# Optimization experiments

Measured on AMD Instinct MI355X. Metric: run time of the kernel, lower is better.

Reference implementation:

```python
import jax, jax.numpy as jnp
import numpy as np

HEADS = 4
DIM_HEAD = 32
DIM = 128
HIDDEN = HEADS * DIM_HEAD  # 128
SCALE = 10
EPS = 1e-12  # matches F.normalize default eps


def l2_norm(t):
    # normalize along last axis (heads axis after the port's reshape)
    n = jnp.sqrt(jnp.sum(t * t, axis=-1, keepdims=True))
    return t / jnp.maximum(n, EPS)


def setup_inputs() -> dict:
    key = jax.random.key(0)
    k1, k2, k3 = jax.random.split(key, 3)
    b, h, w = 4, 16, 256
    x = jax.random.normal(k1, (b, h, w, DIM), dtype=jnp.float32)
    # 1x1 conv kernels collapse to dense matrices on the channel axis
    w_qkv = jax.random.normal(k2, (DIM, 3 * HIDDEN), dtype=jnp.float32) / np.sqrt(DIM).astype(np.float32)
    w_out = jax.random.normal(k3, (HIDDEN, DIM), dtype=jnp.float32) / np.sqrt(HIDDEN).astype(np.float32)
    b_out = jnp.zeros((DIM,), dtype=jnp.float32)
    return {"x": x, "w_qkv": w_qkv, "w_out": w_out, "b_out": b_out}


def reference(x, w_qkv, w_out, b_out):
    b, h, w, c = x.shape
    n = h * w
    # 1x1 conv (no bias) -> qkv, split on channel axis
    qkv = jnp.einsum('bhwc,cf->bhwf', x, w_qkv)
    q, k, v = jnp.split(qkv, 3, axis=-1)
    # faithful port reshape: (b, h, w, hidden) -> (b, dim_head, n, heads)
    q = q.reshape(b, -1, n, HEADS)
    k = k.reshape(b, -1, n, HEADS)
    v = v.reshape(b, -1, n, HEADS)
    q = l2_norm(q)  # computed but unused downstream, as in the source
    k = l2_norm(k)
    # sim: contract over dim_head axis -> (b, n, n, heads)
    sim = jnp.einsum('bhdn,bhen->bden', k, v) * SCALE
    attn = jax.nn.softmax(sim, axis=-2)
    # out: contract attn with v over spatial axis -> (b, n, dim_head, heads)
    out = jnp.einsum('bedh,bndh->benh', attn, v)
    out = out.reshape(b, h, w, HIDDEN)
    # final 1x1 conv with bias
    return jnp.einsum('bhwf,fo->bhwo', out, w_out) + b_out
```

## Files before the change

kernel.cpp:

```cpp
#include <hip/hip_runtime.h>
#include <math.h>


#define SEQ 4096
#define PAIR_ELEMS (SEQ * 32)

typedef __attribute__((ext_vector_type(8))) short bf16x8;
typedef __attribute__((ext_vector_type(4))) float f32x4;

static __device__ __forceinline__ unsigned short f2bf(float x) {
    unsigned u = __float_as_uint(x);
    u += 0x7fffu + ((u >> 16) & 1u);
    return (unsigned short)(u >> 16);
}
static __device__ __forceinline__ float bf2f(unsigned short h) {
    return __uint_as_float(((unsigned)h) << 16);
}

__global__ __launch_bounds__(256) void kv_kernel(const float* __restrict__ x,
                                                 const float* __restrict__ wqkv,
                                                 unsigned short* __restrict__ Qhi,
                                                 unsigned short* __restrict__ Qlo,
                                                 unsigned short* __restrict__ Mhi,
                                                 unsigned short* __restrict__ Mlo,
                                                 unsigned short* __restrict__ Mpv) {
    __shared__ __align__(16) float xs[32][128];
    __shared__ __align__(8) unsigned short vstage[32][128];

    const int b    = blockIdx.x >> 7;
    const int p7   = blockIdx.x & 127;
    const int t    = threadIdx.x;
    const int half = t >> 7;
    const int u    = t & 127;
    const int q    = u & 31;
    const int rg   = u >> 5;
    const int woff = 128 + (half << 7) + (q << 2);

    {
        const float* xb = x + ((size_t)(b * SEQ + p7)) * 128;
#pragma unroll
        for (int uu = 0; uu < 4; ++uu) {
            int idx = t + (uu << 8);
            int j   = idx >> 5;
            int c4  = idx & 31;
            *(float4*)&xs[j][c4 * 4] =
                *(const float4*)(xb + (size_t)j * (128 * 128) + c4 * 4);
        }
    }
    __syncthreads();

    float acc[8][4];
#pragma unroll
    for (int jr = 0; jr < 8; ++jr)
#pragma unroll
        for (int a = 0; a < 4; ++a) acc[jr][a] = 0.f;

    float4 wA[4], wB[4];
#pragma unroll
    for (int i = 0; i < 4; ++i)
        wA[i] = *(const float4*)(wqkv + (size_t)i * 384 + woff);

    auto gstep = [&](float4 (&wcur)[4], float4 (&wnxt)[4], int i4) {
        const int i4n = (i4 + 4) & 127;
#pragma unroll
        for (int i = 0; i < 4; ++i)
            wnxt[i] = *(const float4*)(wqkv + (size_t)(i4n + i) * 384 + woff);
#pragma unroll
        for (int jr = 0; jr < 8; ++jr) {
            float4 xv = *(const float4*)&xs[8 * rg + jr][i4];
            acc[jr][0] = fmaf(xv.x, wcur[0].x, acc[jr][0]);
            acc[jr][1] = fmaf(xv.x, wcur[0].y, acc[jr][1]);
            acc[jr][2] = fmaf(xv.x, wcur[0].z, acc[jr][2]);
            acc[jr][3] = fmaf(xv.x, wcur[0].w, acc[jr][3]);
            acc[jr][0] = fmaf(xv.y, wcur[1].x, acc[jr][0]);
            acc[jr][1] = fmaf(xv.y, wcur[1].y, acc[jr][1]);
            acc[jr][2] = fmaf(xv.y, wcur[1].z, acc[jr][2]);
            acc[jr][3] = fmaf(xv.y, wcur[1].w, acc[jr][3]);
            acc[jr][0] = fmaf(xv.z, wcur[2].x, acc[jr][0]);
            acc[jr][1] = fmaf(xv.z, wcur[2].y, acc[jr][1]);
            acc[jr][2] = fmaf(xv.z, wcur[2].z, acc[jr][2]);
            acc[jr][3] = fmaf(xv.z, wcur[2].w, acc[jr][3]);
            acc[jr][0] = fmaf(xv.w, wcur[3].x, acc[jr][0]);
            acc[jr][1] = fmaf(xv.w, wcur[3].y, acc[jr][1]);
            acc[jr][2] = fmaf(xv.w, wcur[3].z, acc[jr][2]);
            acc[jr][3] = fmaf(xv.w, wcur[3].w, acc[jr][3]);
        }
    };
    for (int i4 = 0; i4 < 128; i4 += 8) {
        gstep(wA, wB, i4);
        gstep(wB, wA, i4 + 4);
    }

    const int pairbase = b << 2;
    const int de = (p7 << 5) + q;

    if (half == 0) {
        float qn[8][4];
#pragma unroll
        for (int jr = 0; jr < 8; ++jr) {
            float s = acc[jr][0] * acc[jr][0] + acc[jr][1] * acc[jr][1]
                    + acc[jr][2] * acc[jr][2] + acc[jr][3] * acc[jr][3];
            float inv = 14.426950408889634f / fmaxf(sqrtf(s), 1e-12f);
#pragma unroll
            for (int a = 0; a < 4; ++a) qn[jr][a] = acc[jr][a] * inv;
        }
#pragma unroll
        for (int a = 0; a < 4; ++a) {
            unsigned hi[4], lo[4];
#pragma unroll
            for (int j2 = 0; j2 < 4; ++j2) {
                float v0 = qn[2 * j2][a], v1 = qn[2 * j2 + 1][a];
                unsigned short h0 = f2bf(v0), h1 = f2bf(v1);
                hi[j2] = (unsigned)h0 | ((unsigned)h1 << 16);
                lo[j2] = (unsigned)f2bf(v0 - bf2f(h0))
                       | ((unsigned)f2bf(v1 - bf2f(h1)) << 16);
            }
            size_t off = (size_t)(pairbase + a) * PAIR_ELEMS + (size_t)de * 32 + 8 * rg;
            *(uint4*)(Qhi + off) = make_uint4(hi[0], hi[1], hi[2], hi[3]);
            *(uint4*)(Qlo + off) = make_uint4(lo[0], lo[1], lo[2], lo[3]);
        }
    } else {
#pragma unroll
        for (int a = 0; a < 4; ++a) {
            unsigned hi[4], lo[4];
#pragma unroll
            for (int j2 = 0; j2 < 4; ++j2) {
                float v0 = acc[2 * j2][a], v1 = acc[2 * j2 + 1][a];
                unsigned short h0 = f2bf(v0), h1 = f2bf(v1);
                hi[j2] = (unsigned)h0 | ((unsigned)h1 << 16);
                lo[j2] = (unsigned)f2bf(v0 - bf2f(h0))
                       | ((unsigned)f2bf(v1 - bf2f(h1)) << 16);
            }
            size_t off = (size_t)(pairbase + a) * PAIR_ELEMS + (size_t)de * 32 + 8 * rg;
            *(uint4*)(Mhi + off) = make_uint4(hi[0], hi[1], hi[2], hi[3]);
            *(uint4*)(Mlo + off) = make_uint4(lo[0], lo[1], lo[2], lo[3]);
        }
#pragma unroll
        for (int jr = 0; jr < 8; ++jr) {
            unsigned short h0 = f2bf(acc[jr][0]);
            unsigned short h1 = f2bf(acc[jr][1]);
            unsigned short h2 = f2bf(acc[jr][2]);
            unsigned short h3 = f2bf(acc[jr][3]);
            *(uint2*)&vstage[8 * rg + jr][4 * q] =
                make_uint2((unsigned)h0 | ((unsigned)h1 << 16),
                           (unsigned)h2 | ((unsigned)h3 << 16));
        }
    }
    __syncthreads();

    unsigned* mpv32 = (unsigned*)Mpv;
#pragma unroll
    for (int uu = 0; uu < 8; ++uu) {
        int task = t + (uu << 8);
        int r  = task & 15;
        int jj = (task >> 4) & 31;
        int aa = task >> 9;
        unsigned lo = vstage[jj][(r << 2) + aa];
        unsigned hi = vstage[jj][(r << 2) + aa + 64];
        int pr = (b << 2) + aa;
        size_t dst = (size_t)pr * (PAIR_ELEMS / 2) + (size_t)jj * (SEQ / 2)
                   + ((size_t)(p7 >> 1) << 5) + (r << 1) + (p7 & 1);
        mpv32[dst] = lo | (hi << 16);
    }
}

__global__ __launch_bounds__(256, 2) void attn_kernel(const unsigned short* __restrict__ Qhi,
                                                      const unsigned short* __restrict__ Qlo,
                                                      const unsigned short* __restrict__ Mhi,
                                                      const unsigned short* __restrict__ Mlo,
                                                      const unsigned short* __restrict__ Mpv,
                                                      unsigned short* __restrict__ outb) {
    __shared__ __align__(16) unsigned short Plds[4][32][72];

    const int bid  = blockIdx.x;
    const int pair = ((bid & 7) << 1) + (bid >> 8);
    const int dblk = (bid & 255) >> 3;
    const int t    = threadIdx.x;
    const int wid  = t >> 6;
    const int lane = t & 63;
    const int col  = lane & 15;
    const int g    = lane >> 4;
    const int d0   = dblk * 128 + wid * 32;

    const size_t pb = (size_t)pair * PAIR_ELEMS;

    bf16x8 ah[2], al[2];
#pragma unroll
    for (int s = 0; s < 2; ++s) {
        size_t o = pb + (size_t)(d0 + 16 * s + col) * 32 + g * 8;
        ah[s] = *(const bf16x8*)(Qhi + o);
        al[s] = *(const bf16x8*)(Qlo + o);
    }

    const unsigned short* mh = Mhi + pb;
    const unsigned short* ml = Mlo + pb;
    const unsigned short* mp = Mpv + pb;
    const f32x4 z = {0.f, 0.f, 0.f, 0.f};

    float rmax[2][4];
#pragma unroll
    for (int s = 0; s < 2; ++s)
#pragma unroll
        for (int r = 0; r < 4; ++r) rmax[s][r] = -3e38f;

    {
        bf16x8 pA[4], pB[4];
#pragma unroll
        for (int cc = 0; cc < 4; ++cc)
            pA[cc] = *(const bf16x8*)(mh + (size_t)(16 * cc + col) * 32 + g * 8);

        auto sweep = [&](bf16x8 (&cur)[4], bf16x8 (&nxt)[4], int e0) {
            const int en = (e0 + 64) & (SEQ - 1);
#pragma unroll
            for (int cc = 0; cc < 4; ++cc)
                nxt[cc] = *(const bf16x8*)(mh + (size_t)(en + 16 * cc + col) * 32 + g * 8);
#pragma unroll
            for (int cc = 0; cc < 4; ++cc) {
#pragma unroll
                for (int s = 0; s < 2; ++s) {
                    f32x4 sv = __builtin_amdgcn_mfma_f32_16x16x32_bf16(ah[s], cur[cc], z, 0, 0, 0);
#pragma unroll
                    for (int r = 0; r < 4; ++r) rmax[s][r] = fmaxf(rmax[s][r], sv[r]);
                }
            }
        };
        for (int e0 = 0; e0 < SEQ; e0 += 128) {
            sweep(pA, pB, e0);
            sweep(pB, pA, e0 + 64);
        }
    }
#pragma unroll
    for (int s = 0; s < 2; ++s)
#pragma unroll
        for (int r = 0; r < 4; ++r) {
            float m = rmax[s][r];
            m = fmaxf(m, __shfl_xor(m, 1));
            m = fmaxf(m, __shfl_xor(m, 2));
            m = fmaxf(m, __shfl_xor(m, 4));
            m = fmaxf(m, __shfl_xor(m, 8));
            rmax[s][r] = m;
        }
    f32x4 minit[2];
#pragma unroll
    for (int s = 0; s < 2; ++s)
        minit[s] = (f32x4){-rmax[s][0], -rmax[s][1], -rmax[s][2], -rmax[s][3]};

    f32x4 O[2][2];
    float lsum[2][4];
#pragma unroll
    for (int s = 0; s < 2; ++s) {
#pragma unroll
        for (int r = 0; r < 4; ++r) lsum[s][r] = 0.f;
#pragma unroll
        for (int nh = 0; nh < 2; ++nh) O[s][nh] = (f32x4){0.f, 0.f, 0.f, 0.f};
    }

    {
        bf16x8 tA[12], tB[12];
#pragma unroll
        for (int cc = 0; cc < 4; ++cc) {
            size_t ro = (size_t)(16 * cc + col) * 32 + g * 8;
            tA[cc]     = *(const bf16x8*)(mh + ro);
            tA[4 + cc] = *(const bf16x8*)(ml + ro);
        }
#pragma unroll
        for (int h = 0; h < 2; ++h)
#pragma unroll
            for (int nh = 0; nh < 2; ++nh)
                tA[8 + 2 * h + nh] =
                    *(const bf16x8*)(mp + (size_t)(16 * nh + col) * SEQ + 32 * h + g * 8);

        auto flash = [&](bf16x8 (&cur)[12], bf16x8 (&nxt)[12], int e0) {
            const int en = (e0 + 64) & (SEQ - 1);
#pragma unroll
            for (int cc = 0; cc < 4; ++cc) {
                size_t ro = (size_t)(en + 16 * cc + col) * 32 + g * 8;
                nxt[cc]     = *(const bf16x8*)(mh + ro);
                nxt[4 + cc] = *(const bf16x8*)(ml + ro);
            }
#pragma unroll
            for (int h = 0; h < 2; ++h)
#pragma unroll
                for (int nh = 0; nh < 2; ++nh)
                    nxt[8 + 2 * h + nh] =
                        *(const bf16x8*)(mp + (size_t)(16 * nh + col) * SEQ
                                         + en + 32 * h + g * 8);

            f32x4 S[2][4];
#pragma unroll
            for (int cc = 0; cc < 4; ++cc) {
#pragma unroll
                for (int s = 0; s < 2; ++s) {
                    f32x4 tac = __builtin_amdgcn_mfma_f32_16x16x32_bf16(ah[s], cur[4 + cc], minit[s], 0, 0, 0);
                    tac = __builtin_amdgcn_mfma_f32_16x16x32_bf16(al[s], cur[cc], tac, 0, 0, 0);
                    S[s][cc] = __builtin_amdgcn_mfma_f32_16x16x32_bf16(ah[s], cur[cc], tac, 0, 0, 0);
                }
            }
#pragma unroll
            for (int s = 0; s < 2; ++s) {
#pragma unroll
                for (int r = 0; r < 4; ++r) {
                    float p0 = __builtin_amdgcn_exp2f(S[s][0][r]);
                    float p1 = __builtin_amdgcn_exp2f(S[s][1][r]);
                    float p2 = __builtin_amdgcn_exp2f(S[s][2][r]);
                    float p3 = __builtin_amdgcn_exp2f(S[s][3][r]);
                    lsum[s][r] += (p0 + p1) + (p2 + p3);
                    unsigned w0 = (unsigned)f2bf(p0) | ((unsigned)f2bf(p1) << 16);
                    unsigned w1 = (unsigned)f2bf(p2) | ((unsigned)f2bf(p3) << 16);
                    unsigned* dst = (unsigned*)&Plds[wid][16 * s + 4 * g + r][col * 4];
                    dst[0] = w0;
                    dst[1] = w1;
                }
            }
            asm volatile("s_waitcnt lgkmcnt(0)" ::: "memory");
            __builtin_amdgcn_sched_barrier(0);
#pragma unroll
            for (int h = 0; h < 2; ++h) {
                bf16x8 pa[2];
#pragma unroll
                for (int s = 0; s < 2; ++s)
                    pa[s] = *(const bf16x8*)&Plds[wid][16 * s + col][32 * h + g * 8];
                O[0][0] = __builtin_amdgcn_mfma_f32_16x16x32_bf16(pa[0], cur[8 + 2 * h + 0], O[0][0], 0, 0, 0);
                O[0][1] = __builtin_amdgcn_mfma_f32_16x16x32_bf16(pa[0], cur[8 + 2 * h + 1], O[0][1], 0, 0, 0);
                O[1][0] = __builtin_amdgcn_mfma_f32_16x16x32_bf16(pa[1], cur[8 + 2 * h + 0], O[1][0], 0, 0, 0);
                O[1][1] = __builtin_amdgcn_mfma_f32_16x16x32_bf16(pa[1], cur[8 + 2 * h + 1], O[1][1], 0, 0, 0);
            }
            asm volatile("" ::: "memory");
        };
        for (int e0 = 0; e0 < SEQ; e0 += 128) {
            flash(tA, tB, e0);
            flash(tB, tA, e0 + 64);
        }
    }

#pragma unroll
    for (int s = 0; s < 2; ++s)
#pragma unroll
        for (int r = 0; r < 4; ++r) {
            float l = lsum[s][r];
            l += __shfl_xor(l, 1);
            l += __shfl_xor(l, 2);
            l += __shfl_xor(l, 4);
            l += __shfl_xor(l, 8);
            lsum[s][r] = l;
        }

    const int bb = pair >> 2;
    const int aa = pair & 3;
#pragma unroll
    for (int s = 0; s < 2; ++s) {
#pragma unroll
        for (int r = 0; r < 4; ++r) {
            int d = d0 + 16 * s + 4 * g + r;
            float inv = 1.0f / lsum[s][r];
#pragma unroll
            for (int nh = 0; nh < 2; ++nh) {
                int n2 = 16 * nh + col;
                outb[((size_t)(bb * SEQ + d)) * 128 + n2 * 4 + aa] =
                    f2bf(O[s][nh][r] * inv);
            }
        }
    }
}

__global__ __launch_bounds__(256) void out_kernel(const unsigned short* __restrict__ opre,
                                                  const float* __restrict__ wout,
                                                  const float* __restrict__ bout,
                                                  float* __restrict__ y) {
    __shared__ __align__(16) float xs[8][128];
    const int r0 = blockIdx.x * 8;
    const int t  = threadIdx.x;
    {
        const unsigned* src = (const unsigned*)(opre + (size_t)r0 * 128);
        unsigned v0 = src[t * 2], v1 = src[t * 2 + 1];
        float* dst = &xs[0][0] + t * 4;
        dst[0] = bf2f((unsigned short)(v0 & 0xffff));
        dst[1] = bf2f((unsigned short)(v0 >> 16));
        dst[2] = bf2f((unsigned short)(v1 & 0xffff));
        dst[3] = bf2f((unsigned short)(v1 >> 16));
    }
    __syncthreads();

    const int c  = t & 127;
    const int rh = (t >> 7) * 4;
    float acc[4] = {0.f, 0.f, 0.f, 0.f};

    for (int i = 0; i < 128; i += 4) {
        float w0 = wout[(i + 0) * 128 + c];
        float w1 = wout[(i + 1) * 128 + c];
        float w2 = wout[(i + 2) * 128 + c];
        float w3 = wout[(i + 3) * 128 + c];
#pragma unroll
        for (int p = 0; p < 4; ++p) {
            float4 xp = *(const float4*)&xs[rh + p][i];
            acc[p] = fmaf(xp.x, w0, acc[p]);
            acc[p] = fmaf(xp.y, w1, acc[p]);
            acc[p] = fmaf(xp.z, w2, acc[p]);
            acc[p] = fmaf(xp.w, w3, acc[p]);
        }
    }
    float bb = bout[c];
#pragma unroll
    for (int p = 0; p < 4; ++p) {
        y[((size_t)(r0 + rh + p)) * 128 + c] = acc[p] + bb;
    }
}

extern "C" void kernel_launch(void* const* d_in, const int* in_sizes, int n_in,
                              void* d_out, int out_size, void* d_ws, size_t ws_size,
                              hipStream_t stream) {
    const float* x    = (const float*)d_in[0];
    const float* wqkv = (const float*)d_in[1];
    const float* wout = (const float*)d_in[2];
    const float* bout = (const float*)d_in[3];
    float* y = (float*)d_out;

    unsigned short* Qhi = (unsigned short*)d_ws;
    unsigned short* Qlo = Qhi + (size_t)16 * PAIR_ELEMS;
    unsigned short* Mhi = Qlo + (size_t)16 * PAIR_ELEMS;
    unsigned short* Mlo = Mhi + (size_t)16 * PAIR_ELEMS;
    unsigned short* Mpv = Mlo + (size_t)16 * PAIR_ELEMS;
    unsigned short* outb = Mpv + (size_t)16 * PAIR_ELEMS;

    kv_kernel<<<512, 256, 0, stream>>>(x, wqkv, Qhi, Qlo, Mhi, Mlo, Mpv);
    attn_kernel<<<512, 256, 0, stream>>>(Qhi, Qlo, Mhi, Mlo, Mpv, outb);
    out_kernel<<<2048, 256, 0, stream>>>(outb, wout, bout, y);
}
```

Before: 259.6 us.

## Transpose score MFMA so P stays in registers, dropping LDS round-trip

The score MFMAs swap their operand order so each lane holds a full column of scores. The exp'd probabilities can then be packed with v_cvt_pk_bf16_f32 and passed straight as the B operand of the PV MFMA, with no LDS staging. To match, the V matrix layout written by kv_kernel is permuted, and the row max and row sum reductions shrink to two cross-group shuffles. The aim is to remove the LDS writes and reads, the lgkmcnt wait and the scheduling barrier from the inner flash loop. The risk is register pressure and getting the permuted layout exactly right.

```diff
diff --git a/kernel.cpp b/kernel.cpp
--- a/kernel.cpp
+++ b/kernel.cpp
@@ -23,7 +23,7 @@
                                                  unsigned short* __restrict__ Qlo,
                                                  unsigned short* __restrict__ Mhi,
                                                  unsigned short* __restrict__ Mlo,
-                                                 unsigned short* __restrict__ Mpv) {
+                                                 unsigned short* __restrict__ Mpv2) {
     __shared__ __align__(16) float xs[32][128];
     __shared__ __align__(8) unsigned short vstage[32][128];
 
@@ -148,18 +148,22 @@
     }
     __syncthreads();
 
-    unsigned* mpv32 = (unsigned*)Mpv;
+    unsigned* mpv32 = (unsigned*)Mpv2;
 #pragma unroll
     for (int uu = 0; uu < 8; ++uu) {
         int task = t + (uu << 8);
-        int r  = task & 15;
+        int w  = task & 15;
         int jj = (task >> 4) & 31;
         int aa = task >> 9;
-        unsigned lo = vstage[jj][(r << 2) + aa];
-        unsigned hi = vstage[jj][(r << 2) + aa + 64];
+        unsigned lo = vstage[jj][(w << 3) + aa];
+        unsigned hi = vstage[jj][(w << 3) + 4 + aa];
         int pr = (b << 2) + aa;
-        size_t dst = (size_t)pr * (PAIR_ELEMS / 2) + (size_t)jj * (SEQ / 2)
-                   + ((size_t)(p7 >> 1) << 5) + (r << 1) + (p7 & 1);
+        size_t dst = (size_t)pr * 65536 + (size_t)jj * 2048
+                   + ((size_t)(p7 >> 1)) * 32
+                   + (size_t)((p7 & 1) * 16)
+                   + (size_t)(((w >> 1) & 3) * 4)
+                   + (size_t)((w >> 3) * 2)
+                   + (size_t)(w & 1);
         mpv32[dst] = lo | (hi << 16);
     }
 }
@@ -168,10 +172,8 @@
                                                       const unsigned short* __restrict__ Qlo,
                                                       const unsigned short* __restrict__ Mhi,
                                                       const unsigned short* __restrict__ Mlo,
-                                                      const unsigned short* __restrict__ Mpv,
+                                                      const unsigned short* __restrict__ Mpv2,
                                                       unsigned short* __restrict__ outb) {
-    __shared__ __align__(16) unsigned short Plds[4][32][72];
-
     const int bid  = blockIdx.x;
     const int pair = ((bid & 7) << 1) + (bid >> 8);
     const int dblk = (bid & 255) >> 3;
@@ -194,15 +196,10 @@
 
     const unsigned short* mh = Mhi + pb;
     const unsigned short* ml = Mlo + pb;
-    const unsigned short* mp = Mpv + pb;
+    const unsigned short* mp = Mpv2 + pb;
     const f32x4 z = {0.f, 0.f, 0.f, 0.f};
 
-    float rmax[2][4];
-#pragma unroll
-    for (int s = 0; s < 2; ++s)
-#pragma unroll
-        for (int r = 0; r < 4; ++r) rmax[s][r] = -3e38f;
-
+    float rmax[2] = {-3e38f, -3e38f};
     {
         bf16x8 pA[4], pB[4];
 #pragma unroll
@@ -218,9 +215,8 @@
             for (int cc = 0; cc < 4; ++cc) {
 #pragma unroll
                 for (int s = 0; s < 2; ++s) {
-                    f32x4 sv = __builtin_amdgcn_mfma_f32_16x16x32_bf16(ah[s], cur[cc], z, 0, 0, 0);
-#pragma unroll
-                    for (int r = 0; r < 4; ++r) rmax[s][r] = fmaxf(rmax[s][r], sv[r]);
+                    f32x4 sv = __builtin_amdgcn_mfma_f32_16x16x32_bf16(cur[cc], ah[s], z, 0, 0, 0);
+                    rmax[s] = fmaxf(rmax[s], fmaxf(fmaxf(sv[0], sv[1]), fmaxf(sv[2], sv[3])));
                 }
             }
         };
@@ -230,30 +226,23 @@
         }
     }
 #pragma unroll
+    for (int s = 0; s < 2; ++s) {
+        float m = rmax[s];
+        m = fmaxf(m, __shfl_xor(m, 16));
+        m = fmaxf(m, __shfl_xor(m, 32));
+        rmax[s] = m;
+    }
+    f32x4 minit[2];
+#pragma unroll
     for (int s = 0; s < 2; ++s)
-#pragma unroll
-        for (int r = 0; r < 4; ++r) {
-            float m = rmax[s][r];
-            m = fmaxf(m, __shfl_xor(m, 1));
-            m = fmaxf(m, __shfl_xor(m, 2));
-            m = fmaxf(m, __shfl_xor(m, 4));
-            m = fmaxf(m, __shfl_xor(m, 8));
-            rmax[s][r] = m;
-        }
-    f32x4 minit[2];
+        minit[s] = (f32x4){-rmax[s], -rmax[s], -rmax[s], -rmax[s]};
+
+    f32x4 O[2][2];
+    float lsum[2] = {0.f, 0.f};
 #pragma unroll
     for (int s = 0; s < 2; ++s)
-        minit[s] = (f32x4){-rmax[s][0], -rmax[s][1], -rmax[s][2], -rmax[s][3]};
-
-    f32x4 O[2][2];
-    float lsum[2][4];
-#pragma unroll
-    for (int s = 0; s < 2; ++s) {
-#pragma unroll
-        for (int r = 0; r < 4; ++r) lsum[s][r] = 0.f;
 #pragma unroll
         for (int nh = 0; nh < 2; ++nh) O[s][nh] = (f32x4){0.f, 0.f, 0.f, 0.f};
-    }
 
     {
         bf16x8 tA[12], tB[12];
@@ -264,11 +253,11 @@
             tA[4 + cc] = *(const bf16x8*)(ml + ro);
         }
 #pragma unroll
-        for (int h = 0; h < 2; ++h)
-#pragma unroll
-            for (int nh = 0; nh < 2; ++nh)
-                tA[8 + 2 * h + nh] =
-                    *(const bf16x8*)(mp + (size_t)(16 * nh + col) * SEQ + 32 * h + g * 8);
+        for (int nh = 0; nh < 2; ++nh)
+#pragma unroll
+            for (int m = 0; m < 2; ++m)
+                tA[8 + 2 * nh + m] =
+                    *(const bf16x8*)(mp + (size_t)(16 * nh + col) * SEQ + 32 * m + 8 * g);
 
         auto flash = [&](bf16x8 (&cur)[12], bf16x8 (&nxt)[12], int e0) {
             const int en = (e0 + 64) & (SEQ - 1);
@@ -279,53 +268,48 @@
                 nxt[4 + cc] = *(const bf16x8*)(ml + ro);
             }
 #pragma unroll
-            for (int h = 0; h < 2; ++h)
-#pragma unroll
-                for (int nh = 0; nh < 2; ++nh)
-                    nxt[8 + 2 * h + nh] =
+            for (int nh = 0; nh < 2; ++nh)
+#pragma unroll
+                for (int m = 0; m < 2; ++m)
+                    nxt[8 + 2 * nh + m] =
                         *(const bf16x8*)(mp + (size_t)(16 * nh + col) * SEQ
-                                         + en + 32 * h + g * 8);
+                                         + en + 32 * m + 8 * g);
 
             f32x4 S[2][4];
 #pragma unroll
             for (int cc = 0; cc < 4; ++cc) {
 #pragma unroll
                 for (int s = 0; s < 2; ++s) {
-                    f32x4 tac = __builtin_amdgcn_mfma_f32_16x16x32_bf16(ah[s], cur[4 + cc], minit[s], 0, 0, 0);
-                    tac = __builtin_amdgcn_mfma_f32_16x16x32_bf16(al[s], cur[cc], tac, 0, 0, 0);
-                    S[s][cc] = __builtin_amdgcn_mfma_f32_16x16x32_bf16(ah[s], cur[cc], tac, 0, 0, 0);
+                    f32x4 tac = __builtin_amdgcn_mfma_f32_16x16x32_bf16(cur[4 + cc], ah[s], minit[s], 0, 0, 0);
+                    tac = __builtin_amdgcn_mfma_f32_16x16x32_bf16(cur[cc], al[s], tac, 0, 0, 0);
+                    S[s][cc] = __builtin_amdgcn_mfma_f32_16x16x32_bf16(cur[cc], ah[s], tac, 0, 0, 0);
                 }
             }
+            unsigned pw[2][4][2];
 #pragma unroll
             for (int s = 0; s < 2; ++s) {
 #pragma unroll
-                for (int r = 0; r < 4; ++r) {
-                    float p0 = __builtin_amdgcn_exp2f(S[s][0][r]);
-                    float p1 = __builtin_amdgcn_exp2f(S[s][1][r]);
-                    float p2 = __builtin_amdgcn_exp2f(S[s][2][r]);
-                    float p3 = __builtin_amdgcn_exp2f(S[s][3][r]);
-                    lsum[s][r] += (p0 + p1) + (p2 + p3);
-                    unsigned w0 = (unsigned)f2bf(p0) | ((unsigned)f2bf(p1) << 16);
-                    unsigned w1 = (unsigned)f2bf(p2) | ((unsigned)f2bf(p3) << 16);
-                    unsigned* dst = (unsigned*)&Plds[wid][16 * s + 4 * g + r][col * 4];
-                    dst[0] = w0;
-                    dst[1] = w1;
+                for (int cc = 0; cc < 4; ++cc) {
+                    float p0 = __builtin_amdgcn_exp2f(S[s][cc][0]);
+                    float p1 = __builtin_amdgcn_exp2f(S[s][cc][1]);
+                    float p2 = __builtin_amdgcn_exp2f(S[s][cc][2]);
+                    float p3 = __builtin_amdgcn_exp2f(S[s][cc][3]);
+                    lsum[s] += (p0 + p1) + (p2 + p3);
+                    asm("v_cvt_pk_bf16_f32 %0, %1, %2" : "=v"(pw[s][cc][0]) : "v"(p0), "v"(p1));
+                    asm("v_cvt_pk_bf16_f32 %0, %1, %2" : "=v"(pw[s][cc][1]) : "v"(p2), "v"(p3));
                 }
             }
-            asm volatile("s_waitcnt lgkmcnt(0)" ::: "memory");
-            __builtin_amdgcn_sched_barrier(0);
-#pragma unroll
-            for (int h = 0; h < 2; ++h) {
-                bf16x8 pa[2];
-#pragma unroll
-                for (int s = 0; s < 2; ++s)
-                    pa[s] = *(const bf16x8*)&Plds[wid][16 * s + col][32 * h + g * 8];
-                O[0][0] = __builtin_amdgcn_mfma_f32_16x16x32_bf16(pa[0], cur[8 + 2 * h + 0], O[0][0], 0, 0, 0);
-                O[0][1] = __builtin_amdgcn_mfma_f32_16x16x32_bf16(pa[0], cur[8 + 2 * h + 1], O[0][1], 0, 0, 0);
-                O[1][0] = __builtin_amdgcn_mfma_f32_16x16x32_bf16(pa[1], cur[8 + 2 * h + 0], O[1][0], 0, 0, 0);
-                O[1][1] = __builtin_amdgcn_mfma_f32_16x16x32_bf16(pa[1], cur[8 + 2 * h + 1], O[1][1], 0, 0, 0);
-            }
-            asm volatile("" ::: "memory");
+#pragma unroll
+            for (int s = 0; s < 2; ++s) {
+#pragma unroll
+                for (int m = 0; m < 2; ++m) {
+                    unsigned pk4[4] = {pw[s][2 * m][0], pw[s][2 * m][1],
+                                       pw[s][2 * m + 1][0], pw[s][2 * m + 1][1]};
+                    bf16x8 pbf = *(bf16x8*)pk4;
+                    O[s][0] = __builtin_amdgcn_mfma_f32_16x16x32_bf16(cur[8 + 0 + m], pbf, O[s][0], 0, 0, 0);
+                    O[s][1] = __builtin_amdgcn_mfma_f32_16x16x32_bf16(cur[8 + 2 + m], pbf, O[s][1], 0, 0, 0);
+                }
+            }
         };
         for (int e0 = 0; e0 < SEQ; e0 += 128) {
             flash(tA, tB, e0);
@@ -334,30 +318,25 @@
     }
 
 #pragma unroll
-    for (int s = 0; s < 2; ++s)
-#pragma unroll
-        for (int r = 0; r < 4; ++r) {
-            float l = lsum[s][r];
-            l += __shfl_xor(l, 1);
-            l += __shfl_xor(l, 2);
-            l += __shfl_xor(l, 4);
-            l += __shfl_xor(l, 8);
-            lsum[s][r] = l;
-        }
+    for (int s = 0; s < 2; ++s) {
+        float l = lsum[s];
+        l += __shfl_xor(l, 16);
+        l += __shfl_xor(l, 32);
+        lsum[s] = l;
+    }
 
     const int bb = pair >> 2;
     const int aa = pair & 3;
 #pragma unroll
     for (int s = 0; s < 2; ++s) {
-#pragma unroll
-        for (int r = 0; r < 4; ++r) {
-            int d = d0 + 16 * s + 4 * g + r;
-            float inv = 1.0f / lsum[s][r];
-#pragma unroll
-            for (int nh = 0; nh < 2; ++nh) {
-                int n2 = 16 * nh + col;
-                outb[((size_t)(bb * SEQ + d)) * 128 + n2 * 4 + aa] =
-                    f2bf(O[s][nh][r] * inv);
+        float inv = 1.0f / lsum[s];
+        size_t rowb = ((size_t)(bb * SEQ + d0 + 16 * s + col)) * 128;
+#pragma unroll
+        for (int nh = 0; nh < 2; ++nh) {
+#pragma unroll
+            for (int r = 0; r < 4; ++r) {
+                int n = 16 * nh + 4 * g + r;
+                outb[rowb + n * 4 + aa] = f2bf(O[s][nh][r] * inv);
             }
         }
     }
@@ -419,10 +398,10 @@
     unsigned short* Qlo = Qhi + (size_t)16 * PAIR_ELEMS;
     unsigned short* Mhi = Qlo + (size_t)16 * PAIR_ELEMS;
     unsigned short* Mlo = Mhi + (size_t)16 * PAIR_ELEMS;
-    unsigned short* Mpv = Mlo + (size_t)16 * PAIR_ELEMS;
-    unsigned short* outb = Mpv + (size_t)16 * PAIR_ELEMS;
-
-    kv_kernel<<<512, 256, 0, stream>>>(x, wqkv, Qhi, Qlo, Mhi, Mlo, Mpv);
-    attn_kernel<<<512, 256, 0, stream>>>(Qhi, Qlo, Mhi, Mlo, Mpv, outb);
+    unsigned short* Mpv2 = Mlo + (size_t)16 * PAIR_ELEMS;
+    unsigned short* outb = Mpv2 + (size_t)16 * PAIR_ELEMS;
+
+    kv_kernel<<<512, 256, 0, stream>>>(x, wqkv, Qhi, Qlo, Mhi, Mlo, Mpv2);
+    attn_kernel<<<512, 256, 0, stream>>>(Qhi, Qlo, Mhi, Mlo, Mpv2, outb);
     out_kernel<<<2048, 256, 0, stream>>>(outb, wout, bout, y);
 }
```

New measurement: 270.3 us. 1.04x slower.
